# Kernel optimization log

Measured on AMD Instinct MI355X. Metric: run time of the kernel, lower is better.

## Reference

```python
import jax, jax.numpy as jnp
import numpy as np

B, D, H, W, C = 4, 8, 56, 56, 128
NH = 4
WS = (2, 7, 7)   # window size (d, h, w)
SS = (1, 3, 3)   # shift size
HD = C // NH
MLP_HIDDEN = 4 * C


def _window_partition(x, ws):
    # x: (b, d, h, w, c) -> (b*nW, wd*wh*ww, c)
    b, d, h, w, c = x.shape
    wd, wh, ww = ws
    x = x.reshape(b, d // wd, wd, h // wh, wh, w // ww, ww, c)
    return x.transpose(0, 1, 3, 5, 2, 4, 6, 7).reshape(-1, wd * wh * ww, c)


def _window_reverse(win, ws, b, d, h, w):
    wd, wh, ww = ws
    x = win.reshape(b, d // wd, h // wh, w // ww, wd, wh, ww, -1)
    return x.transpose(0, 1, 4, 2, 5, 3, 6, 7).reshape(b, d, h, w, -1)


def _layernorm(x, g, b, eps=1e-5):
    mu = jnp.mean(x, axis=-1, keepdims=True)
    var = jnp.var(x, axis=-1, keepdims=True)
    return (x - mu) * jax.lax.rsqrt(var + eps) * g + b


def setup_inputs() -> dict:
    key = jax.random.key(0)
    ks = jax.random.split(key, 10)
    wd, wh, ww = WS
    sd, sh, sw = SS
    N = wd * wh * ww

    x = jax.random.normal(ks[0], (B, D, H, W, C), jnp.float32)

    # ---- attention mask for cyclic shift (compute_mask) ----
    img = np.zeros((1, D, H, W, 1), np.float32)
    cnt = 0
    for dsl in (slice(0, -wd), slice(-wd, -sd), slice(-sd, None)):
        for hsl in (slice(0, -wh), slice(-wh, -sh), slice(-sh, None)):
            for wsl in (slice(0, -ww), slice(-ww, -sw), slice(-sw, None)):
                img[:, dsl, hsl, wsl, :] = cnt
                cnt += 1
    mw = img.reshape(1, D // wd, wd, H // wh, wh, W // ww, ww, 1)
    mw = mw.transpose(0, 1, 3, 5, 2, 4, 6, 7).reshape(-1, N)  # (nW, N)
    am = mw[:, None, :] - mw[:, :, None]
    mask = jnp.asarray(np.where(am != 0, -100.0, 0.0).astype(np.float32))

    # ---- relative position index (buffer) ----
    coords = np.stack(np.meshgrid(np.arange(wd), np.arange(wh), np.arange(ww),
                                  indexing='ij')).reshape(3, -1)
    rel = (coords[:, :, None] - coords[:, None, :]).transpose(1, 2, 0)
    rel[..., 0] += wd - 1
    rel[..., 1] += wh - 1
    rel[..., 2] += ww - 1
    rel[..., 0] *= (2 * wh - 1) * (2 * ww - 1)
    rel[..., 1] *= (2 * ww - 1)
    rel_index = jnp.asarray(rel.sum(-1).astype(np.int32))  # (N, N)

    s = 0.02
    n_bias = (2 * wd - 1) * (2 * wh - 1) * (2 * ww - 1)
    return {
        'x': x,
        'mask': mask,
        'rel_index': rel_index,
        'norm1_g': jnp.ones((C,), jnp.float32),
        'norm1_b': jnp.zeros((C,), jnp.float32),
        'qkv_w': s * jax.random.normal(ks[1], (3 * C, C), jnp.float32),
        'qkv_b': jnp.zeros((3 * C,), jnp.float32),
        'rpb': s * jax.random.normal(ks[2], (n_bias, NH), jnp.float32),
        'proj_w': s * jax.random.normal(ks[3], (C, C), jnp.float32),
        'proj_b': jnp.zeros((C,), jnp.float32),
        'norm2_g': jnp.ones((C,), jnp.float32),
        'norm2_b': jnp.zeros((C,), jnp.float32),
        'fc1_w': s * jax.random.normal(ks[4], (MLP_HIDDEN, C), jnp.float32),
        'fc1_b': jnp.zeros((MLP_HIDDEN,), jnp.float32),
        'fc2_w': s * jax.random.normal(ks[5], (C, MLP_HIDDEN), jnp.float32),
        'fc2_b': jnp.zeros((C,), jnp.float32),
    }


def reference(x, mask, rel_index, norm1_g, norm1_b, qkv_w, qkv_b, rpb,
              proj_w, proj_b, norm2_g, norm2_b, fc1_w, fc1_b, fc2_w, fc2_b):
    shortcut = x
    # ---- part1: norm -> shift -> window attention -> reverse ----
    y = _layernorm(x, norm1_g, norm1_b)
    # dims divisible by window: no padding. Cyclic shift.
    y = jnp.roll(y, (-SS[0], -SS[1], -SS[2]), axis=(1, 2, 3))
    xw = _window_partition(y, WS)                      # (Bn, N, C)
    Bn, N, _ = xw.shape
    qkv = xw @ qkv_w.T + qkv_b                         # (Bn, N, 3C)
    qkv = qkv.reshape(Bn, N, 3, NH, HD).transpose(2, 0, 3, 1, 4)
    q = qkv[0] * (HD ** -0.5)
    k, v = qkv[1], qkv[2]
    attn = jnp.einsum('bhnd,bhmd->bhnm', q, k)         # (Bn, NH, N, N)
    bias = rpb[rel_index.reshape(-1)].reshape(N, N, NH).transpose(2, 0, 1)
    attn = attn + bias[None]
    nW = mask.shape[0]
    attn = attn.reshape(Bn // nW, nW, NH, N, N) + mask[None, :, None]
    attn = jax.nn.softmax(attn, axis=-1).reshape(Bn, NH, N, N)
    out = jnp.einsum('bhnm,bhmd->bhnd', attn, v)
    out = out.transpose(0, 2, 1, 3).reshape(Bn, N, C)
    out = out @ proj_w.T + proj_b
    y = _window_reverse(out, WS, B, D, H, W)
    y = jnp.roll(y, SS, axis=(1, 2, 3))
    x = shortcut + y
    # ---- part2: MLP ----
    h1 = _layernorm(x, norm2_g, norm2_b)
    h1 = jax.nn.gelu(h1 @ fc1_w.T + fc1_b, approximate=False)
    x = x + (h1 @ fc2_w.T + fc2_b)
    return x
```

## Files before the change

### kernel.cpp

```cpp
#include <hip/hip_runtime.h>
#include <hip/hip_bf16.h>
#include <math.h>

using bf16 = __hip_bfloat16;
typedef __attribute__((ext_vector_type(8))) short short8;
typedef __attribute__((ext_vector_type(4))) float float4v;
typedef __attribute__((ext_vector_type(4))) unsigned short ushort4v;

#define DEVI __device__ __forceinline__

constexpr int Nc = 98;
constexpr int NWIN = 256;
constexpr int BNc = 4 * NWIN;
constexpr int NTOK = 4 * 8 * 56 * 56;

DEVI float b2f(bf16 v) { return __bfloat162float(v); }
DEVI short f2bs(float v) { bf16 h = __float2bfloat16(v); return *reinterpret_cast<short*>(&h); }

DEVI float4v mfma16(short8 a, short8 b, float4v c) {
    return __builtin_amdgcn_mfma_f32_16x16x32_bf16(a, b, c, 0, 0, 0);
}

DEVI float gelu_tanh(float x) {
    float t = 0.7978845608028654f * (x + 0.044715f * x * x * x);
    float at = fabsf(t);
    float e2 = __expf(-2.0f * at);
    float th = (1.0f - e2) / (1.0f + e2);
    th = copysignf(th, t);
    return 0.5f * x * (1.0f + th);
}

DEVI void gload16(const short* g, short* lds_base) {
    __builtin_amdgcn_global_load_lds((const __attribute__((address_space(1))) unsigned int*)g,
                                     (__attribute__((address_space(3))) unsigned int*)lds_base,
                                     16, 0, 0);
}

__global__ __launch_bounds__(256) void k_wconv(const float* __restrict__ qw, const float* __restrict__ pw,
                                               const float* __restrict__ f1, const float* __restrict__ f2,
                                               short* __restrict__ wbf) {
    int i = blockIdx.x * 256 + threadIdx.x;
    float v;
    if (i < 49152) v = qw[i];
    else if (i < 65536) v = pw[i - 49152];
    else if (i < 131072) v = f1[i - 65536];
    else v = f2[i - 131072];
    wbf[i] = f2bs(v);
}

__global__ __launch_bounds__(256) void k_cmb(const int* __restrict__ relidx, const float* __restrict__ rpb,
                                             const float* __restrict__ mask, short* __restrict__ cmbT) {
    int elem = blockIdx.x * 256 + threadIdx.x;
    int sl = blockIdx.y;
    int wc = sl >> 2, head = sl & 3;
    int j = elem / 112, i = elem - j * 112;
    float v;
    if (j >= 98)      v = -1e30f;
    else if (i >= 98) v = 0.f;
    else              v = rpb[relidx[i * 98 + j] * 4 + head] + mask[(size_t)wc * 9604 + i * 98 + j];
    cmbT[(size_t)sl * 12544 + elem] = f2bs(v);
}

__global__ __launch_bounds__(256) void k_ln1_win(const float* __restrict__ x,
                                                 const float* __restrict__ g,
                                                 const float* __restrict__ bta,
                                                 bf16* __restrict__ xw) {
    int wave = (blockIdx.x * 256 + threadIdx.x) >> 6;
    int lane = threadIdx.x & 63;
    int win = wave / Nc, n = wave % Nc;
    int bb = win >> 8;
    int rem = win & 255;
    int dblk = rem >> 6, hblk = (rem >> 3) & 7, wblk = rem & 7;
    int wd = n / 49, r49 = n % 49, wh = r49 / 7, ww = r49 % 7;
    int d = dblk * 2 + wd, h = hblk * 7 + wh, w = wblk * 7 + ww;
    int ds = d + 1;  if (ds >= 8)  ds -= 8;
    int hs = h + 3;  if (hs >= 56) hs -= 56;
    int wsp = w + 3; if (wsp >= 56) wsp -= 56;
    size_t src = ((((size_t)bb * 8 + ds) * 56 + hs) * 56 + wsp) * 128;
    int c = lane * 2;
    float2 v = *reinterpret_cast<const float2*>(x + src + c);
    float v0 = v.x, v1 = v.y;
    float s = v0 + v1, sq = v0 * v0 + v1 * v1;
    #pragma unroll
    for (int off = 32; off; off >>= 1) { s += __shfl_xor(s, off); sq += __shfl_xor(sq, off); }
    float mean = s * (1.0f / 128.0f);
    float var  = sq * (1.0f / 128.0f) - mean * mean;
    float inv  = rsqrtf(var + 1e-5f);
    size_t dst = (size_t)wave * 128 + c;
    xw[dst]     = __float2bfloat16((v0 - mean) * inv * g[c]     + bta[c]);
    xw[dst + 1] = __float2bfloat16((v1 - mean) * inv * g[c + 1] + bta[c + 1]);
}

template<int K, int EPI, typename OutT>
__global__ __launch_bounds__(256) void k_gemm_mfma(const short* __restrict__ A,
                                                   const short* __restrict__ Bw,
                                                   const float* __restrict__ bias,
                                                   const float* __restrict__ res,
                                                   OutT* __restrict__ out, int Ncols) {
    __shared__ __align__(16) short smem[128 * 136];
    short* sA = smem;
    short* sB = smem + 8192;
    int t = threadIdx.x;
    int lane = t & 63, wid = t >> 6;
    int wm = wid >> 1, wn = wid & 1;
    int rsub = lane >> 3;
    int csl  = lane & 7;
    int m0 = blockIdx.x * 128, n0 = blockIdx.y * 128;
    float4v acc[4][4];
    #pragma unroll
    for (int a = 0; a < 4; ++a)
        #pragma unroll
        for (int b = 0; b < 4; ++b) acc[a][b] = (float4v){0.f, 0.f, 0.f, 0.f};

    for (int k0 = 0; k0 < K; k0 += 64) {
        #pragma unroll
        for (int v = 0; v < 4; ++v) {
            int row = (wid * 4 + v) * 8 + rsub;
            int ch = csl ^ (row & 7);
            gload16(A + (size_t)(m0 + row) * K + k0 + ch * 8, sA + (wid * 4 + v) * 512);
            gload16(Bw + (size_t)(n0 + row) * K + k0 + ch * 8, sB + (wid * 4 + v) * 512);
        }
        __syncthreads();
        #pragma unroll
        for (int kk = 0; kk < 2; ++kk) {
            int crb = kk * 4 + (lane >> 4);
            short8 af[4], bfr[4];
            #pragma unroll
            for (int mf = 0; mf < 4; ++mf) {
                int row = wm * 64 + mf * 16 + (lane & 15);
                af[mf] = *reinterpret_cast<const short8*>(&sA[row * 64 + (crb ^ (row & 7)) * 8]);
            }
            #pragma unroll
            for (int nf = 0; nf < 4; ++nf) {
                int row = wn * 64 + nf * 16 + (lane & 15);
                bfr[nf] = *reinterpret_cast<const short8*>(&sB[row * 64 + (crb ^ (row & 7)) * 8]);
            }
            #pragma unroll
            for (int mf = 0; mf < 4; ++mf)
                #pragma unroll
                for (int nf = 0; nf < 4; ++nf)
                    acc[mf][nf] = mfma16(af[mf], bfr[nf], acc[mf][nf]);
        }
        __syncthreads();
    }
    if constexpr (sizeof(OutT) == 2) {
        #pragma unroll
        for (int nf = 0; nf < 4; ++nf) {
            int col = wn * 64 + nf * 16 + (lane & 15);
            int gcol = n0 + col;
            float bv = bias[gcol];
            #pragma unroll
            for (int mf = 0; mf < 4; ++mf) {
                #pragma unroll
                for (int r = 0; r < 4; ++r) {
                    int row = wm * 64 + mf * 16 + (lane >> 4) * 4 + r;
                    float v = acc[mf][nf][r] + bv;
                    if (EPI == 0) { if (gcol < 128) v *= 0.17677669529663689f; }
                    else if (EPI == 2) { v = gelu_tanh(v); }
                    smem[row * 136 + col] = f2bs(v);
                }
            }
        }
        __syncthreads();
        #pragma unroll
        for (int p = 0; p < 8; ++p) {
            int row = p * 16 + (t >> 4);
            int c0 = (t & 15) * 8;
            uint4 val = *reinterpret_cast<const uint4*>(&smem[row * 136 + c0]);
            *reinterpret_cast<uint4*>(out + (size_t)(m0 + row) * Ncols + n0 + c0) = val;
        }
    } else {
        #pragma unroll
        for (int mf = 0; mf < 4; ++mf) {
            #pragma unroll
            for (int nf = 0; nf < 4; ++nf) {
                int col = n0 + wn * 64 + nf * 16 + (lane & 15);
                float bv = bias[col];
                #pragma unroll
                for (int r = 0; r < 4; ++r) {
                    size_t row = m0 + wm * 64 + mf * 16 + (lane >> 4) * 4 + r;
                    float v = acc[mf][nf][r] + bv;
                    if (EPI == 3) v += res[row * 128 + col];
                    out[row * Ncols + col] = v;
                }
            }
        }
    }
}

__global__ __launch_bounds__(256) void k_proj_fused(const short* __restrict__ A,
                                                    const short* __restrict__ Bw,
                                                    const float* __restrict__ bias,
                                                    const float* __restrict__ x,
                                                    const float* __restrict__ g,
                                                    const float* __restrict__ bta,
                                                    float* __restrict__ x1,
                                                    bf16* __restrict__ xn2) {
    __shared__ __align__(16) short smem[128 * 136];
    short* sA = smem;
    short* sB = smem + 8192;
    int t = threadIdx.x;
    int lane = t & 63, wid = t >> 6;
    int wm = wid >> 1, wn = wid & 1;
    int rsub = lane >> 3, csl = lane & 7;
    int m0 = blockIdx.x * 128;
    float4v acc[4][4];
    #pragma unroll
    for (int a = 0; a < 4; ++a)
        #pragma unroll
        for (int b = 0; b < 4; ++b) acc[a][b] = (float4v){0.f, 0.f, 0.f, 0.f};

    for (int k0 = 0; k0 < 128; k0 += 64) {
        #pragma unroll
        for (int v = 0; v < 4; ++v) {
            int row = (wid * 4 + v) * 8 + rsub;
            int ch = csl ^ (row & 7);
            gload16(A + (size_t)(m0 + row) * 128 + k0 + ch * 8, sA + (wid * 4 + v) * 512);
            gload16(Bw + (size_t)row * 128 + k0 + ch * 8, sB + (wid * 4 + v) * 512);
        }
        __syncthreads();
        #pragma unroll
        for (int kk = 0; kk < 2; ++kk) {
            int crb = kk * 4 + (lane >> 4);
            short8 af[4], bfr[4];
            #pragma unroll
            for (int mf = 0; mf < 4; ++mf) {
                int row = wm * 64 + mf * 16 + (lane & 15);
                af[mf] = *reinterpret_cast<const short8*>(&sA[row * 64 + (crb ^ (row & 7)) * 8]);
            }
            #pragma unroll
            for (int nf = 0; nf < 4; ++nf) {
                int row = wn * 64 + nf * 16 + (lane & 15);
                bfr[nf] = *reinterpret_cast<const short8*>(&sB[row * 64 + (crb ^ (row & 7)) * 8]);
            }
            #pragma unroll
            for (int mf = 0; mf < 4; ++mf)
                #pragma unroll
                for (int nf = 0; nf < 4; ++nf)
                    acc[mf][nf] = mfma16(af[mf], bfr[nf], acc[mf][nf]);
        }
        __syncthreads();
    }

    int*   tokmap = (int*)smem;
    float* psum   = (float*)(smem + 256);
    float* psq    = (float*)(smem + 768);
    if (t < 128) {
        int wr = m0 + t;
        int win = wr / 98, n = wr - win * 98;
        int bb = win >> 8, rem = win & 255;
        int dblk = rem >> 6, hblk = (rem >> 3) & 7, wblk = rem & 7;
        int wd = n / 49, r49 = n - wd * 49, wh = r49 / 7, ww = r49 - wh * 7;
        int d = dblk * 2 + wd, h = hblk * 7 + wh, w = wblk * 7 + ww;
        int dd = d + 1;  if (dd >= 8)  dd -= 8;
        int hh = h + 3;  if (hh >= 56) hh -= 56;
        int w2 = w + 3;  if (w2 >= 56) w2 -= 56;
        tokmap[t] = ((bb * 8 + dd) * 56 + hh) * 56 + w2;
    }
    __syncthreads();

    #pragma unroll
    for (int mf = 0; mf < 4; ++mf) {
        #pragma unroll
        for (int r = 0; r < 4; ++r) {
            int row = wm * 64 + mf * 16 + (lane >> 4) * 4 + r;
            int tok = tokmap[row];
            float s = 0.f, sq = 0.f;
            #pragma unroll
            for (int nf = 0; nf < 4; ++nf) {
                int col = wn * 64 + nf * 16 + (lane & 15);
                float vv = acc[mf][nf][r] + bias[col] + x[(size_t)tok * 128 + col];
                acc[mf][nf][r] = vv;
                s += vv; sq += vv * vv;
            }
            #pragma unroll
            for (int m = 1; m <= 8; m <<= 1) { s += __shfl_xor(s, m); sq += __shfl_xor(sq, m); }
            if ((lane & 15) == 0) { psum[row * 2 + wn] = s; psq[row * 2 + wn] = sq; }
        }
    }
    __syncthreads();
    #pragma unroll
    for (int mf = 0; mf < 4; ++mf) {
        #pragma unroll
        for (int r = 0; r < 4; ++r) {
            int row = wm * 64 + mf * 16 + (lane >> 4) * 4 + r;
            int tok = tokmap[row];
            float s  = psum[row * 2] + psum[row * 2 + 1];
            float sq = psq[row * 2]  + psq[row * 2 + 1];
            float mean = s * (1.0f / 128.0f);
            float var  = sq * (1.0f / 128.0f) - mean * mean;
            float inv  = rsqrtf(var + 1e-5f);
            #pragma unroll
            for (int nf = 0; nf < 4; ++nf) {
                int col = wn * 64 + nf * 16 + (lane & 15);
                float vv = acc[mf][nf][r];
                x1[(size_t)tok * 128 + col] = vv;
                xn2[(size_t)tok * 128 + col] = __float2bfloat16((vv - mean) * inv * g[col] + bta[col]);
            }
        }
    }
}

__global__ __launch_bounds__(256, 4) void k_attn_mfma(const bf16* __restrict__ qkv,
                                                      const short* __restrict__ cmbT,
                                                      bf16* __restrict__ aout) {
    constexpr int QP = 40;
    constexpr int VP = 136;
    constexpr int PP = 136;
    __shared__ __align__(16) char smem[8704 + 30464];
    short* sVT = (short*)smem;
    short* sQ  = (short*)(smem + 8704);
    short* sK  = (short*)(smem + 8704 + 8960);
    short* sP  = (short*)(smem + 8704);
    int t = threadIdx.x, lane = t & 63, wid = t >> 6;
    int win = blockIdx.x >> 2, head = blockIdx.x & 3;
    const bf16* base = qkv + (size_t)win * Nc * 384 + head * 32;

    for (int idx = t; idx < Nc * 4; idx += 256) {
        int i = idx >> 2, g = idx & 3;
        uint4 q4 = *reinterpret_cast<const uint4*>(base + (size_t)i * 384 + g * 8);
        uint4 k4 = *reinterpret_cast<const uint4*>(base + (size_t)i * 384 + 128 + g * 8);
        uint4 v4 = *reinterpret_cast<const uint4*>(base + (size_t)i * 384 + 256 + g * 8);
        *reinterpret_cast<uint4*>(&sQ[i * QP + g * 8]) = q4;
        *reinterpret_cast<uint4*>(&sK[i * QP + g * 8]) = k4;
        const short* vp = reinterpret_cast<const short*>(&v4);
        #pragma unroll
        for (int e = 0; e < 8; ++e) sVT[(g * 8 + e) * VP + i] = vp[e];
    }
    for (int idx = t; idx < 14 * QP; idx += 256) {
        int r = 98 + idx / QP, c = idx % QP;
        sQ[r * QP + c] = 0; sK[r * QP + c] = 0;
    }
    for (int idx = t; idx < 32 * 30; idx += 256) {
        int d = idx / 30, c = 98 + idx % 30;
        sVT[d * VP + c] = 0;
    }
    __syncthreads();

    float4v s[2][7];
    #pragma unroll
    for (int mi = 0; mi < 2; ++mi)
        #pragma unroll
        for (int fn = 0; fn < 7; ++fn) s[mi][fn] = (float4v){0.f, 0.f, 0.f, 0.f};
    short8 qf[2];
    #pragma unroll
    for (int mi = 0; mi < 2; ++mi) {
        if (wid * 2 + mi < 7) {
            int row = (wid * 2 + mi) * 16 + (lane & 15);
            qf[mi] = *reinterpret_cast<const short8*>(&sQ[row * QP + (lane >> 4) * 8]);
        }
    }
    #pragma unroll
    for (int fn = 0; fn < 7; ++fn) {
        short8 kf = *reinterpret_cast<const short8*>(&sK[(fn * 16 + (lane & 15)) * QP + (lane >> 4) * 8]);
        #pragma unroll
        for (int mi = 0; mi < 2; ++mi) {
            if (wid * 2 + mi < 7) s[mi][fn] = mfma16(qf[mi], kf, s[mi][fn]);
        }
    }

    const unsigned short* cb = (const unsigned short*)(cmbT + (size_t)((win & 255) * 4 + head) * 12544);
    #pragma unroll
    for (int mi = 0; mi < 2; ++mi) {
        if (wid * 2 + mi >= 7) continue;
        int i0 = (wid * 2 + mi) * 16 + (lane >> 4) * 4;
        #pragma unroll
        for (int fn = 0; fn < 7; ++fn) {
            int j = fn * 16 + (lane & 15);
            ushort4v bm4 = *reinterpret_cast<const ushort4v*>(cb + j * 112 + i0);
            #pragma unroll
            for (int r = 0; r < 4; ++r) {
                union { unsigned u; float f; } cv; cv.u = ((unsigned)bm4[r]) << 16;
                s[mi][fn][r] = __expf(s[mi][fn][r] + cv.f);
            }
        }
        #pragma unroll
        for (int r = 0; r < 4; ++r) {
            float sum = 0.f;
            #pragma unroll
            for (int fn = 0; fn < 7; ++fn) sum += s[mi][fn][r];
            #pragma unroll
            for (int m = 1; m <= 8; m <<= 1) sum += __shfl_xor(sum, m);
            float inv = 1.0f / sum;
            #pragma unroll
            for (int fn = 0; fn < 7; ++fn) s[mi][fn][r] *= inv;
        }
    }
    __syncthreads();

    for (int idx = t; idx < 112 * 16; idx += 256) {
        int rr = idx >> 4, c2 = 112 + (idx & 15);
        sP[rr * PP + c2] = 0;
    }
    #pragma unroll
    for (int mi = 0; mi < 2; ++mi) {
        if (wid * 2 + mi >= 7) continue;
        int i0 = (wid * 2 + mi) * 16 + (lane >> 4) * 4;
        #pragma unroll
        for (int r = 0; r < 4; ++r) {
            #pragma unroll
            for (int fn = 0; fn < 7; ++fn) {
                int j = fn * 16 + (lane & 15);
                sP[(i0 + r) * PP + j] = f2bs(s[mi][fn][r]);
            }
        }
    }
    __syncthreads();

    float4v o[2][2];
    #pragma unroll
    for (int mi = 0; mi < 2; ++mi)
        #pragma unroll
        for (int nd = 0; nd < 2; ++nd) o[mi][nd] = (float4v){0.f, 0.f, 0.f, 0.f};
    #pragma unroll
    for (int jc = 0; jc < 4; ++jc) {
        short8 pf[2];
        #pragma unroll
        for (int mi = 0; mi < 2; ++mi) {
            if (wid * 2 + mi < 7) {
                int row = (wid * 2 + mi) * 16 + (lane & 15);
                pf[mi] = *reinterpret_cast<const short8*>(&sP[row * PP + jc * 32 + (lane >> 4) * 8]);
            }
        }
        #pragma unroll
        for (int nd = 0; nd < 2; ++nd) {
            short8 vf = *reinterpret_cast<const short8*>(&sVT[(nd * 16 + (lane & 15)) * VP + jc * 32 + (lane >> 4) * 8]);
            #pragma unroll
            for (int mi = 0; mi < 2; ++mi) {
                if (wid * 2 + mi < 7) o[mi][nd] = mfma16(pf[mi], vf, o[mi][nd]);
            }
        }
    }
    bf16* obase = aout + (size_t)win * Nc * 128 + head * 32;
    #pragma unroll
    for (int mi = 0; mi < 2; ++mi) {
        if (wid * 2 + mi >= 7) continue;
        #pragma unroll
        for (int nd = 0; nd < 2; ++nd) {
            int d = nd * 16 + (lane & 15);
            #pragma unroll
            for (int r = 0; r < 4; ++r) {
                int i = (wid * 2 + mi) * 16 + (lane >> 4) * 4 + r;
                if (i < 98) obase[(size_t)i * 128 + d] = __float2bfloat16(o[mi][nd][r]);
            }
        }
    }
}

extern "C" void kernel_launch(void* const* d_in, const int* in_sizes, int n_in,
                              void* d_out, int out_size, void* d_ws, size_t ws_size,
                              hipStream_t stream) {
    const float* x      = (const float*)d_in[0];
    const float* mask   = (const float*)d_in[1];
    const int*   relidx = (const int*)  d_in[2];
    const float* n1g    = (const float*)d_in[3];
    const float* n1b    = (const float*)d_in[4];
    const float* qkv_w  = (const float*)d_in[5];
    const float* qkv_b  = (const float*)d_in[6];
    const float* rpb    = (const float*)d_in[7];
    const float* proj_w = (const float*)d_in[8];
    const float* proj_b = (const float*)d_in[9];
    const float* n2g    = (const float*)d_in[10];
    const float* n2b    = (const float*)d_in[11];
    const float* fc1_w  = (const float*)d_in[12];
    const float* fc1_b  = (const float*)d_in[13];
    const float* fc2_w  = (const float*)d_in[14];
    const float* fc2_b  = (const float*)d_in[15];

    char* ws = (char*)d_ws;
    const size_t MB = 1024 * 1024;
    bf16*  xw   = (bf16*)(ws);
    bf16*  qkv  = (bf16*)(ws + 25 * MB);
    bf16*  aout = (bf16*)(ws + 99 * MB);
    short* cmbT = (short*)(ws + 149 * MB);
    float* x1   = (float*)(ws);
    bf16*  xn2  = (bf16*)(ws + 50 * MB);
    bf16*  h1   = (bf16*)(ws + 75 * MB);
    short* wbf  = (short*)(ws + 174 * MB);
    float* out  = (float*)d_out;

    const short* wq = wbf;
    const short* wp = wbf + 49152;
    const short* w1 = wbf + 65536;
    const short* w2 = wbf + 131072;

    k_wconv<<<768, 256, 0, stream>>>(qkv_w, proj_w, fc1_w, fc2_w, wbf);
    k_cmb<<<dim3(49, 1024), 256, 0, stream>>>(relidx, rpb, mask, cmbT);
    k_ln1_win<<<NTOK / 4, 256, 0, stream>>>(x, n1g, n1b, xw);
    k_gemm_mfma<128, 0, bf16><<<dim3(NTOK / 128, 3), 256, 0, stream>>>((const short*)xw, wq, qkv_b, nullptr, qkv, 384);
    k_attn_mfma<<<BNc * 4, 256, 0, stream>>>(qkv, cmbT, aout);
    k_proj_fused<<<NTOK / 128, 256, 0, stream>>>((const short*)aout, wp, proj_b, x, n2g, n2b, x1, xn2);
    k_gemm_mfma<128, 2, bf16><<<dim3(NTOK / 128, 4), 256, 0, stream>>>((const short*)xn2, w1, fc1_b, nullptr, h1, 512);
    k_gemm_mfma<512, 3, float><<<dim3(NTOK / 128, 1), 256, 0, stream>>>((const short*)h1, w2, fc2_b, x1, out, 128);
}
```

Baseline: 282.5 us.

## Add weight-stationary persistent GEMM with double-buffered A tiles for QKV and FC1

Adds a GEMM kernel for K=128 that loads its 128x128 weight slice once into registers. Each block then loops over several 64-row A tiles, prefetching two tiles ahead into double-buffered LDS with async global loads and explicit waitcnt and barrier control. This is meant to remove repeated weight loads and overlap A-tile fetches with MFMA work. The old bf16 epilogue path in the generic GEMM is dropped because only the fp32 FC2 path still uses it. Fewer, longer-lived blocks and more LDS per block may lower occupancy, and the hand-tuned vmcnt counts depend on the exact load count per thread.

After: 293.4 us. 3.9% more time.

```diff
diff --git a/kernel.cpp b/kernel.cpp
--- a/kernel.cpp
+++ b/kernel.cpp
@@ -91,6 +91,129 @@
     xw[dst + 1] = __float2bfloat16((v1 - mean) * inv * g[c + 1] + bta[c + 1]);
 }
 
+template<int EPI, int T>
+__global__ __launch_bounds__(256) void k_gemm_ws(const short* __restrict__ A,
+                                                 const short* __restrict__ Bw,
+                                                 const float* __restrict__ bias,
+                                                 bf16* __restrict__ out, int Ncols) {
+    __shared__ __align__(16) short sW[128 * 128];
+    __shared__ __align__(16) short sA[2][64 * 128];
+    __shared__ __align__(16) short sC[64 * 128];
+    int t = threadIdx.x, lane = t & 63, wid = t >> 6;
+    int wr = wid >> 1, wc = wid & 1;
+    int n0 = blockIdx.y * 128;
+    size_t mbase = (size_t)blockIdx.x * T * 64;
+
+    #pragma unroll
+    for (int v = 0; v < 8; ++v) {
+        int u = v * 256 + wid * 64 + lane;
+        int row = u >> 4, csl = u & 15;
+        gload16(Bw + (size_t)(n0 + row) * 128 + (csl ^ (row & 7)) * 8,
+                sW + (v * 256 + wid * 64) * 8);
+    }
+    #pragma unroll
+    for (int b = 0; b < 2; ++b) {
+        #pragma unroll
+        for (int v = 0; v < 4; ++v) {
+            int u = v * 256 + wid * 64 + lane;
+            int row = u >> 4, csl = u & 15;
+            gload16(A + (mbase + (size_t)b * 64 + row) * 128 + (csl ^ (row & 7)) * 8,
+                    sA[b] + (v * 256 + wid * 64) * 8);
+        }
+    }
+    asm volatile("s_waitcnt vmcnt(8)" ::: "memory");
+    __builtin_amdgcn_sched_barrier(0);
+    __builtin_amdgcn_s_barrier();
+    __builtin_amdgcn_sched_barrier(0);
+
+    short8 wf[4][4];
+    float bv[4];
+    #pragma unroll
+    for (int nf = 0; nf < 4; ++nf) {
+        int row = wc * 64 + nf * 16 + (lane & 15);
+        bv[nf] = bias[n0 + row];
+        #pragma unroll
+        for (int kc = 0; kc < 4; ++kc)
+            wf[nf][kc] = *reinterpret_cast<const short8*>(
+                &sW[row * 128 + ((kc * 4 + (lane >> 4)) ^ (row & 7)) * 8]);
+    }
+
+    for (int i = 0; i < T; ++i) {
+        if (i == 0)                     { asm volatile("s_waitcnt vmcnt(4)" ::: "memory"); }
+        else if (i == 1 || i == T - 1)  { asm volatile("s_waitcnt vmcnt(8)" ::: "memory"); }
+        else                            { asm volatile("s_waitcnt vmcnt(12)" ::: "memory"); }
+        __builtin_amdgcn_sched_barrier(0);
+        __builtin_amdgcn_s_barrier();
+        __builtin_amdgcn_sched_barrier(0);
+
+        const short* buf = sA[i & 1];
+        short8 af[2][4];
+        #pragma unroll
+        for (int mf = 0; mf < 2; ++mf) {
+            int row = wr * 32 + mf * 16 + (lane & 15);
+            #pragma unroll
+            for (int kc = 0; kc < 4; ++kc)
+                af[mf][kc] = *reinterpret_cast<const short8*>(
+                    &buf[row * 128 + ((kc * 4 + (lane >> 4)) ^ (row & 7)) * 8]);
+        }
+        asm volatile("s_waitcnt lgkmcnt(0)" ::: "memory");
+        __builtin_amdgcn_sched_barrier(0);
+        __builtin_amdgcn_s_barrier();
+        __builtin_amdgcn_sched_barrier(0);
+
+        if (i + 2 < T) {
+            #pragma unroll
+            for (int v = 0; v < 4; ++v) {
+                int u = v * 256 + wid * 64 + lane;
+                int row = u >> 4, csl = u & 15;
+                gload16(A + (mbase + (size_t)(i + 2) * 64 + row) * 128 + (csl ^ (row & 7)) * 8,
+                        sA[i & 1] + (v * 256 + wid * 64) * 8);
+            }
+        }
+
+        float4v acc[2][4];
+        #pragma unroll
+        for (int mf = 0; mf < 2; ++mf)
+            #pragma unroll
+            for (int nf = 0; nf < 4; ++nf) acc[mf][nf] = (float4v){0.f, 0.f, 0.f, 0.f};
+        #pragma unroll
+        for (int kc = 0; kc < 4; ++kc)
+            #pragma unroll
+            for (int mf = 0; mf < 2; ++mf)
+                #pragma unroll
+                for (int nf = 0; nf < 4; ++nf)
+                    acc[mf][nf] = mfma16(af[mf][kc], wf[nf][kc], acc[mf][nf]);
+
+        #pragma unroll
+        for (int mf = 0; mf < 2; ++mf) {
+            #pragma unroll
+            for (int nf = 0; nf < 4; ++nf) {
+                int col = wc * 64 + nf * 16 + (lane & 15);
+                #pragma unroll
+                for (int r = 0; r < 4; ++r) {
+                    int row = wr * 32 + mf * 16 + (lane >> 4) * 4 + r;
+                    float v = acc[mf][nf][r] + bv[nf];
+                    if (EPI == 0) { if (blockIdx.y == 0) v *= 0.17677669529663689f; }
+                    else if (EPI == 2) { v = gelu_tanh(v); }
+                    sC[row * 128 + col] = f2bs(v);
+                }
+            }
+        }
+        asm volatile("s_waitcnt lgkmcnt(0)" ::: "memory");
+        __builtin_amdgcn_sched_barrier(0);
+        __builtin_amdgcn_s_barrier();
+        __builtin_amdgcn_sched_barrier(0);
+        size_t m0 = mbase + (size_t)i * 64;
+        #pragma unroll
+        for (int p = 0; p < 4; ++p) {
+            int u = t + p * 256;
+            int row = u >> 4, c8 = u & 15;
+            uint4 val = *reinterpret_cast<const uint4*>(&sC[row * 128 + c8 * 8]);
+            *reinterpret_cast<uint4*>(out + (m0 + row) * Ncols + n0 + c8 * 8) = val;
+        }
+    }
+}
+
 template<int K, int EPI, typename OutT>
 __global__ __launch_bounds__(256) void k_gemm_mfma(const short* __restrict__ A,
                                                    const short* __restrict__ Bw,
@@ -143,46 +266,18 @@
         }
         __syncthreads();
     }
-    if constexpr (sizeof(OutT) == 2) {
+    #pragma unroll
+    for (int mf = 0; mf < 4; ++mf) {
         #pragma unroll
         for (int nf = 0; nf < 4; ++nf) {
-            int col = wn * 64 + nf * 16 + (lane & 15);
-            int gcol = n0 + col;
-            float bv = bias[gcol];
-            #pragma unroll
-            for (int mf = 0; mf < 4; ++mf) {
-                #pragma unroll
-                for (int r = 0; r < 4; ++r) {
-                    int row = wm * 64 + mf * 16 + (lane >> 4) * 4 + r;
-                    float v = acc[mf][nf][r] + bv;
-                    if (EPI == 0) { if (gcol < 128) v *= 0.17677669529663689f; }
-                    else if (EPI == 2) { v = gelu_tanh(v); }
-                    smem[row * 136 + col] = f2bs(v);
-                }
-            }
-        }
-        __syncthreads();
-        #pragma unroll
-        for (int p = 0; p < 8; ++p) {
-            int row = p * 16 + (t >> 4);
-            int c0 = (t & 15) * 8;
-            uint4 val = *reinterpret_cast<const uint4*>(&smem[row * 136 + c0]);
-            *reinterpret_cast<uint4*>(out + (size_t)(m0 + row) * Ncols + n0 + c0) = val;
-        }
-    } else {
-        #pragma unroll
-        for (int mf = 0; mf < 4; ++mf) {
-            #pragma unroll
-            for (int nf = 0; nf < 4; ++nf) {
-                int col = n0 + wn * 64 + nf * 16 + (lane & 15);
-                float bv = bias[col];
-                #pragma unroll
-                for (int r = 0; r < 4; ++r) {
-                    size_t row = m0 + wm * 64 + mf * 16 + (lane >> 4) * 4 + r;
-                    float v = acc[mf][nf][r] + bv;
-                    if (EPI == 3) v += res[row * 128 + col];
-                    out[row * Ncols + col] = v;
-                }
+            int col = n0 + wn * 64 + nf * 16 + (lane & 15);
+            float bvv = bias[col];
+            #pragma unroll
+            for (int r = 0; r < 4; ++r) {
+                size_t row = m0 + wm * 64 + mf * 16 + (lane >> 4) * 4 + r;
+                float v = acc[mf][nf][r] + bvv;
+                if (EPI == 3) v += res[row * 128 + col];
+                out[row * Ncols + col] = v;
             }
         }
     }
@@ -246,8 +341,8 @@
     float* psum   = (float*)(smem + 256);
     float* psq    = (float*)(smem + 768);
     if (t < 128) {
-        int wr = m0 + t;
-        int win = wr / 98, n = wr - win * 98;
+        int wr2 = m0 + t;
+        int win = wr2 / 98, n = wr2 - win * 98;
         int bb = win >> 8, rem = win & 255;
         int dblk = rem >> 6, hblk = (rem >> 3) & 7, wblk = rem & 7;
         int wd = n / 49, r49 = n - wd * 49, wh = r49 / 7, ww = r49 - wh * 7;
@@ -487,9 +582,9 @@
     k_wconv<<<768, 256, 0, stream>>>(qkv_w, proj_w, fc1_w, fc2_w, wbf);
     k_cmb<<<dim3(49, 1024), 256, 0, stream>>>(relidx, rpb, mask, cmbT);
     k_ln1_win<<<NTOK / 4, 256, 0, stream>>>(x, n1g, n1b, xw);
-    k_gemm_mfma<128, 0, bf16><<<dim3(NTOK / 128, 3), 256, 0, stream>>>((const short*)xw, wq, qkv_b, nullptr, qkv, 384);
+    k_gemm_ws<0, 4><<<dim3(392, 3), 256, 0, stream>>>((const short*)xw, wq, qkv_b, qkv, 384);
     k_attn_mfma<<<BNc * 4, 256, 0, stream>>>(qkv, cmbT, aout);
     k_proj_fused<<<NTOK / 128, 256, 0, stream>>>((const short*)aout, wp, proj_b, x, n2g, n2b, x1, xn2);
-    k_gemm_mfma<128, 2, bf16><<<dim3(NTOK / 128, 4), 256, 0, stream>>>((const short*)xn2, w1, fc1_b, nullptr, h1, 512);
+    k_gemm_ws<2, 8><<<dim3(196, 4), 256, 0, stream>>>((const short*)xn2, w1, fc1_b, h1, 512);
     k_gemm_mfma<512, 3, float><<<dim3(NTOK / 128, 1), 256, 0, stream>>>((const short*)h1, w2, fc2_b, x1, out, 128);
 }
```
